# Kernel tuning notes

Measured on AMD Instinct MI355X. Metric: run time of the kernel, lower is better.

Reference implementation:

```python
import jax, jax.numpy as jnp
import numpy as np

NEG_SLOPE = 0.2  # GAT LeakyReLU slope
NEG_INF = -1e9


def setup_inputs() -> dict:
    key = jax.random.key(0)
    ks = jax.random.split(key, 5)
    B, N, D = 16, 1024, 256
    H, F = 4, 64  # heads, per-head out dim (out_dim=256)
    x = jax.random.normal(ks[0], (B, N, D), dtype=jnp.float32)
    adj = jax.random.uniform(ks[1], (B, N, N), dtype=jnp.float32)
    W = jax.random.normal(ks[2], (D, H * F), dtype=jnp.float32) * (1.0 / np.sqrt(D))
    a_src = jax.random.normal(ks[3], (H, F), dtype=jnp.float32) * (1.0 / np.sqrt(F))
    a_dst = jax.random.normal(ks[4], (H, F), dtype=jnp.float32) * (1.0 / np.sqrt(F))
    bias = jnp.zeros((H * F,), dtype=jnp.float32)
    return {"x": x, "adj": adj, "W": W, "a_src": a_src, "a_dst": a_dst, "bias": bias}


def reference(x, adj, W, a_src, a_dst, bias):
    B, N, D = x.shape
    H, F = a_src.shape
    # Linear transform per head: [B,N,H,F]
    h = jnp.einsum("bnd,dhf->bnhf", x, W.reshape(D, H, F))
    # Attention logit components: [B,N,H]
    e_src = jnp.einsum("bnhf,hf->bnh", h, a_src)
    e_dst = jnp.einsum("bnhf,hf->bnh", h, a_dst)
    # logits[b,i,j,h]: target i gathers from source j (edge = adj[b,i,j] > 0.5)
    logits = e_dst[:, :, None, :] + e_src[:, None, :, :]
    logits = jnp.where(logits >= 0, logits, NEG_SLOPE * logits)  # LeakyReLU
    mask = adj > 0.5  # [B,N,N]
    logits = jnp.where(mask[..., None], logits, NEG_INF)
    att = jax.nn.softmax(logits, axis=2)  # softmax over source neighbors j
    out = jnp.einsum("bijh,bjhf->bihf", att, h)  # aggregate
    return out.reshape(B, N, H * F) + bias  # concat heads
```

## Files before the change

### kernel.cpp

```cpp
#include <hip/hip_runtime.h>

typedef __bf16 bf16x8 __attribute__((ext_vector_type(8)));
typedef float f32x4 __attribute__((ext_vector_type(4)));

constexpr int Bsz = 16;
constexpr int Nsz = 1024;
constexpr int Dsz = 256;
constexpr int Hsz = 4;
constexpr int HFsz = 256;
constexpr int BN = Bsz * Nsz;
constexpr float LOG2E = 1.44269504088896340736f;

__device__ __forceinline__ unsigned f2bf(float f) {
    unsigned u = __float_as_uint(f);
    return (u + 0x7FFFu + ((u >> 16) & 1u)) >> 16;
}

__global__ __launch_bounds__(256) void wcvt(const float* __restrict__ Wm,
                                            unsigned short* __restrict__ WbT) {
    const int t = threadIdx.x;
    const int c = blockIdx.x * 4 + (t >> 6);
    const int d0 = (t & 63) * 4;
    const float v0 = Wm[(size_t)(d0 + 0) * HFsz + c];
    const float v1 = Wm[(size_t)(d0 + 1) * HFsz + c];
    const float v2 = Wm[(size_t)(d0 + 2) * HFsz + c];
    const float v3 = Wm[(size_t)(d0 + 3) * HFsz + c];
    uint2 pk;
    pk.x = f2bf(v0) | (f2bf(v1) << 16);
    pk.y = f2bf(v2) | (f2bf(v3) << 16);
    *(uint2*)&WbT[(size_t)c * Dsz + d0] = pk;
}

__global__ __launch_bounds__(256) void gat_h_e3(
    const float* __restrict__ x,
    const unsigned short* __restrict__ WbT,
    const float* __restrict__ a_src,
    const float* __restrict__ a_dst,
    unsigned short* __restrict__ hT,
    float* __restrict__ esrcT,
    float* __restrict__ edstT)
{
    const int n0g = blockIdx.x * 32, b = n0g >> 10, n0 = n0g & 1023;
    const int t = threadIdx.x, lane = t & 63, w = t >> 6;
    const int m = lane & 15, q = lane >> 4;

    __shared__ alignas(16) unsigned short Lds[4 * 64 * 40];

    const float4* x4 = (const float4*)(x + (size_t)n0g * Dsz);
#pragma unroll
    for (int i = 0; i < 8; ++i) {
        const int f = t + 256 * i;
        const int row = f >> 6, d4 = (f & 63) * 4;
        const float4 xv = x4[f];
        uint2 pk;
        pk.x = f2bf(xv.x) | (f2bf(xv.y) << 16);
        pk.y = f2bf(xv.z) | (f2bf(xv.w) << 16);
        *(uint2*)&Lds[row * 264 + d4] = pk;
    }
    __syncthreads();

    const unsigned short* Ab = WbT + (size_t)(w * 64 + m) * Dsz + q * 8;
    f32x4 acc[4][2];
#pragma unroll
    for (int ht = 0; ht < 4; ++ht)
#pragma unroll
        for (int nt = 0; nt < 2; ++nt) acc[ht][nt] = (f32x4){0.f, 0.f, 0.f, 0.f};

#pragma unroll
    for (int kk = 0; kk < 8; ++kk) {
        const int k0 = kk * 32;
        const bf16x8 bfr0 = *(const bf16x8*)&Lds[(0 * 16 + m) * 264 + k0 + q * 8];
        const bf16x8 bfr1 = *(const bf16x8*)&Lds[(1 * 16 + m) * 264 + k0 + q * 8];
#pragma unroll
        for (int ht = 0; ht < 4; ++ht) {
            const bf16x8 afr = *(const bf16x8*)&Ab[ht * 16 * Dsz + k0];
            acc[ht][0] = __builtin_amdgcn_mfma_f32_16x16x32_bf16(afr, bfr0, acc[ht][0], 0, 0, 0);
            acc[ht][1] = __builtin_amdgcn_mfma_f32_16x16x32_bf16(afr, bfr1, acc[ht][1], 0, 0, 0);
        }
    }

    float ps0 = 0.f, ps1 = 0.f, pd0 = 0.f, pd1 = 0.f;
#pragma unroll
    for (int ht = 0; ht < 4; ++ht)
#pragma unroll
        for (int r = 0; r < 4; ++r) {
            const float as = a_src[w * 64 + ht * 16 + q * 4 + r];
            const float ad = a_dst[w * 64 + ht * 16 + q * 4 + r];
            ps0 += acc[ht][0][r] * as;  ps1 += acc[ht][1][r] * as;
            pd0 += acc[ht][0][r] * ad;  pd1 += acc[ht][1][r] * ad;
        }
    ps0 += __shfl_xor(ps0, 16, 64); ps0 += __shfl_xor(ps0, 32, 64);
    ps1 += __shfl_xor(ps1, 16, 64); ps1 += __shfl_xor(ps1, 32, 64);
    pd0 += __shfl_xor(pd0, 16, 64); pd0 += __shfl_xor(pd0, 32, 64);
    pd1 += __shfl_xor(pd1, 16, 64); pd1 += __shfl_xor(pd1, 32, 64);
    if (q == 0) {
        const size_t eb = (size_t)(b * Hsz + w) * Nsz + n0;
        esrcT[eb + m]      = ps0 * LOG2E;  esrcT[eb + 16 + m] = ps1 * LOG2E;
        edstT[eb + m]      = pd0 * LOG2E;  edstT[eb + 16 + m] = pd1 * LOG2E;
    }

    __syncthreads();

#pragma unroll
    for (int ht = 0; ht < 4; ++ht)
#pragma unroll
        for (int r = 0; r < 4; ++r) {
            const int hf = ht * 16 + q * 4 + r;
            Lds[w * 2560 + hf * 40 + m]      = (unsigned short)f2bf(acc[ht][0][r]);
            Lds[w * 2560 + hf * 40 + 16 + m] = (unsigned short)f2bf(acc[ht][1][r]);
        }
#pragma unroll
    for (int s = 0; s < 4; ++s) {
        const int hf = s * 16 + (lane >> 2), ck = lane & 3;
        const bf16x8 hv = *(const bf16x8*)&Lds[w * 2560 + hf * 40 + ck * 8];
        *(bf16x8*)&hT[(size_t)(b * HFsz + w * 64 + hf) * Nsz + n0 + ck * 8] = hv;
    }
}

__device__ __forceinline__ unsigned pexp2(float ed, float e0, float e1,
                                          float a0, float a1) {
    float v0 = ed + e0, v1 = ed + e1;
    v0 = fmaxf(v0, 0.2f * v0);
    v1 = fmaxf(v1, 0.2f * v1);
    float p0, p1;
    asm("v_exp_f32 %0, %1" : "=v"(p0) : "v"(v0));
    asm("v_exp_f32 %0, %1" : "=v"(p1) : "v"(v1));
    unsigned u0 = __float_as_uint(p0), u1 = __float_as_uint(p1);
    u0 = (a0 > 0.5f) ? u0 : 0u;
    u1 = (a1 > 0.5f) ? u1 : 0u;
    return (u0 >> 16) | (u1 & 0xFFFF0000u);
}

__global__ __launch_bounds__(256, 6) void gat_attn6(
    const float* __restrict__ adj,
    const unsigned short* __restrict__ hT,
    const float* __restrict__ esrcT,
    const float* __restrict__ edstT,
    const float* __restrict__ bias,
    float* __restrict__ outp)
{
    const int gid = blockIdx.x;
    const int b  = gid & 15;
    const int hw = (gid >> 4) & 3;
    const int i0 = (gid >> 6) * 16;
    const int t = threadIdx.x;
    const int lane = t & 63, ws = t >> 6;
    const int m = lane & 15, q = lane >> 4;

    __shared__ alignas(16) float comb[4 * 64 * 20];

    const float* adjr = adj + (size_t)b * Nsz * Nsz + (size_t)(i0 + m) * Nsz;
    const float* esb  = esrcT + (size_t)(b * Hsz + hw) * Nsz;
    const float ed_s  = edstT[(size_t)(b * Hsz + hw) * Nsz + i0 + m];
    const unsigned short* hTb = hT + (size_t)(b * HFsz + hw * 64 + m) * Nsz + q * 8;

    bf16x8 ones;
#pragma unroll
    for (int i = 0; i < 8; ++i)
        ((unsigned short*)&ones)[i] = 0x3F80;

    f32x4 acc[4];
#pragma unroll
    for (int nt = 0; nt < 4; ++nt) acc[nt] = (f32x4){0.f, 0.f, 0.f, 0.f};
    f32x4 acc5 = (f32x4){0.f, 0.f, 0.f, 0.f};

#pragma unroll 1
    for (int jt = 0; jt < 4; ++jt) {
        const int j0 = (ws * 4 + jt) * 64;
#pragma unroll
        for (int kk = 0; kk < 2; ++kk) {
            const int jc = j0 + kk * 32 + q * 8;
            const float4 a0 = *(const float4*)&adjr[jc];
            const float4 a1 = *(const float4*)&adjr[jc + 4];
            const float4 e0 = *(const float4*)&esb[jc];
            const float4 e1 = *(const float4*)&esb[jc + 4];
            bf16x8 bfr[4];
#pragma unroll
            for (int nt = 0; nt < 4; ++nt)
                bfr[nt] = *(const bf16x8*)&hTb[(size_t)nt * 16 * Nsz + j0 + kk * 32];

            union { unsigned u[4]; bf16x8 v; } af;
            af.u[0] = pexp2(ed_s, e0.x, e0.y, a0.x, a0.y);
            af.u[1] = pexp2(ed_s, e0.z, e0.w, a0.z, a0.w);
            af.u[2] = pexp2(ed_s, e1.x, e1.y, a1.x, a1.y);
            af.u[3] = pexp2(ed_s, e1.z, e1.w, a1.z, a1.w);

#pragma unroll
            for (int nt = 0; nt < 4; ++nt)
                acc[nt] = __builtin_amdgcn_mfma_f32_16x16x32_bf16(
                    af.v, bfr[nt], acc[nt], 0, 0, 0);
            acc5 = __builtin_amdgcn_mfma_f32_16x16x32_bf16(af.v, ones, acc5,
                                                           0, 0, 0);
        }
    }

    __syncthreads();
    {
        float* cw = comb + (ws * 64 + lane) * 20;
#pragma unroll
        for (int nt = 0; nt < 4; ++nt)
#pragma unroll
            for (int r = 0; r < 4; ++r) cw[nt * 4 + r] = acc[nt][r];
#pragma unroll
        for (int r = 0; r < 4; ++r) cw[16 + r] = acc5[r];
    }
    __syncthreads();

    const int row = t >> 4, c4 = t & 15;
    const int rq = row >> 2, rr = row & 3;
    const int nt4 = (c4 >> 2) * 4;
    const int mb = (c4 & 3) * 4;
    float n0 = 0.f, n1 = 0.f, n2 = 0.f, n3 = 0.f, den = 0.f;
#pragma unroll
    for (int w4 = 0; w4 < 4; ++w4) {
        const float* cb = comb + (w4 * 64 + rq * 16) * 20;
        den += cb[16 + rr];
        n0 += cb[(mb + 0) * 20 + nt4 + rr];
        n1 += cb[(mb + 1) * 20 + nt4 + rr];
        n2 += cb[(mb + 2) * 20 + nt4 + rr];
        n3 += cb[(mb + 3) * 20 + nt4 + rr];
    }
    const float inv = 1.f / den;
    const float4 b4 = *(const float4*)&bias[hw * 64 + c4 * 4];
    float4 o;
    o.x = n0 * inv + b4.x;  o.y = n1 * inv + b4.y;
    o.z = n2 * inv + b4.z;  o.w = n3 * inv + b4.w;
    *(float4*)&outp[(size_t)(b * Nsz + i0 + row) * HFsz + hw * 64 + c4 * 4] = o;
}

extern "C" void kernel_launch(void* const* d_in, const int* in_sizes, int n_in,
                              void* d_out, int out_size, void* d_ws, size_t ws_size,
                              hipStream_t stream) {
    const float* x     = (const float*)d_in[0];
    const float* adj   = (const float*)d_in[1];
    const float* Wm    = (const float*)d_in[2];
    const float* a_src = (const float*)d_in[3];
    const float* a_dst = (const float*)d_in[4];
    const float* bias  = (const float*)d_in[5];
    float* outp = (float*)d_out;

    unsigned short* hT  = (unsigned short*)d_ws;
    unsigned short* WbT = hT + (size_t)BN * HFsz;
    float* esrcT = (float*)(WbT + (size_t)HFsz * Dsz);
    float* edstT = esrcT + (size_t)Bsz * Hsz * Nsz;

    wcvt<<<dim3(64), dim3(256), 0, stream>>>(Wm, WbT);
    gat_h_e3<<<dim3(BN / 32), dim3(256), 0, stream>>>(x, WbT, a_src, a_dst,
                                                      hT, esrcT, edstT);
    gat_attn6<<<dim3(4096), dim3(256), 0, stream>>>(adj, hT, esrcT, edstT,
                                                    bias, outp);
}
```

Before: 212.7 us.

## Share adjacency tiles across heads via double-buffered LDS in 512-thread blocks

Each block now covers all four heads for a 16-row tile, using 8 waves (4 heads by 2 j-halves) instead of one block per head. Adjacency rows are loaded once into double-buffered shared memory and reused by the four head waves, so adj traffic from global memory drops to a quarter. The cost is two barriers per j-tile, a larger LDS footprint and bigger blocks, which may lower occupancy and add synchronisation stalls.

```diff
diff --git a/kernel.cpp b/kernel.cpp
--- a/kernel.cpp
+++ b/kernel.cpp
@@ -131,7 +131,7 @@
     return (u0 >> 16) | (u1 & 0xFFFF0000u);
 }
 
-__global__ __launch_bounds__(256, 6) void gat_attn6(
+__global__ __launch_bounds__(512, 6) void gat_attn7(
     const float* __restrict__ adj,
     const unsigned short* __restrict__ hT,
     const float* __restrict__ esrcT,
@@ -141,18 +141,23 @@
 {
     const int gid = blockIdx.x;
     const int b  = gid & 15;
-    const int hw = (gid >> 4) & 3;
-    const int i0 = (gid >> 6) * 16;
+    const int i0 = (gid >> 4) * 16;
     const int t = threadIdx.x;
     const int lane = t & 63, ws = t >> 6;
+    const int hh = ws & 3, jh = ws >> 2;
     const int m = lane & 15, q = lane >> 4;
 
-    __shared__ alignas(16) float comb[4 * 64 * 20];
-
-    const float* adjr = adj + (size_t)b * Nsz * Nsz + (size_t)(i0 + m) * Nsz;
-    const float* esb  = esrcT + (size_t)(b * Hsz + hw) * Nsz;
-    const float ed_s  = edstT[(size_t)(b * Hsz + hw) * Nsz + i0 + m];
-    const unsigned short* hTb = hT + (size_t)(b * HFsz + hw * 64 + m) * Nsz + q * 8;
+    __shared__ alignas(16) float smem[10240];
+
+    const float* adjSg = adj + (size_t)b * Nsz * Nsz
+                             + (size_t)(i0 + hh * 4 + q) * Nsz + m * 4;
+    float* stW = &smem[(jh * 2) * 1088 + (hh * 4 + q) * 68 + m * 4];
+    const float* stR = &smem[(jh * 2) * 1088 + m * 68];
+
+    const float* esb = esrcT + (size_t)(b * Hsz + hh) * Nsz;
+    const float ed_s = edstT[(size_t)(b * Hsz + hh) * Nsz + i0 + m];
+    const unsigned short* hTb = hT + (size_t)(b * HFsz + hh * 64 + m) * Nsz + q * 8;
+    const int jt0 = jh * 8;
 
     bf16x8 ones;
 #pragma unroll
@@ -164,14 +169,26 @@
     for (int nt = 0; nt < 4; ++nt) acc[nt] = (f32x4){0.f, 0.f, 0.f, 0.f};
     f32x4 acc5 = (f32x4){0.f, 0.f, 0.f, 0.f};
 
+    {
+        const float4 g = *(const float4*)&adjSg[jt0 * 64];
+        *(float4*)&stW[0] = g;
+    }
+    __syncthreads();
+
 #pragma unroll 1
-    for (int jt = 0; jt < 4; ++jt) {
-        const int j0 = (ws * 4 + jt) * 64;
+    for (int jl = 0; jl < 8; ++jl) {
+        const int buf = jl & 1;
+        const int j0 = (jt0 + jl) * 64;
+
+        float4 g;
+        if (jl < 7) g = *(const float4*)&adjSg[(jt0 + jl + 1) * 64];
+
+        const float* rd = stR + buf * 1088;
 #pragma unroll
         for (int kk = 0; kk < 2; ++kk) {
             const int jc = j0 + kk * 32 + q * 8;
-            const float4 a0 = *(const float4*)&adjr[jc];
-            const float4 a1 = *(const float4*)&adjr[jc + 4];
+            const float4 a0 = *(const float4*)&rd[kk * 32 + q * 8];
+            const float4 a1 = *(const float4*)&rd[kk * 32 + q * 8 + 4];
             const float4 e0 = *(const float4*)&esb[jc];
             const float4 e1 = *(const float4*)&esb[jc + 4];
             bf16x8 bfr[4];
@@ -192,11 +209,14 @@
             acc5 = __builtin_amdgcn_mfma_f32_16x16x32_bf16(af.v, ones, acc5,
                                                            0, 0, 0);
         }
-    }
-
-    __syncthreads();
+
+        __syncthreads();
+        if (jl < 7) *(float4*)&stW[(buf ^ 1) * 1088] = g;
+        __syncthreads();
+    }
+
     {
-        float* cw = comb + (ws * 64 + lane) * 20;
+        float* cw = &smem[t * 20];
 #pragma unroll
         for (int nt = 0; nt < 4; ++nt)
 #pragma unroll
@@ -206,26 +226,30 @@
     }
     __syncthreads();
 
-    const int row = t >> 4, c4 = t & 15;
-    const int rq = row >> 2, rr = row & 3;
-    const int nt4 = (c4 >> 2) * 4;
-    const int mb = (c4 & 3) * 4;
-    float n0 = 0.f, n1 = 0.f, n2 = 0.f, n3 = 0.f, den = 0.f;
-#pragma unroll
-    for (int w4 = 0; w4 < 4; ++w4) {
-        const float* cb = comb + (w4 * 64 + rq * 16) * 20;
-        den += cb[16 + rr];
-        n0 += cb[(mb + 0) * 20 + nt4 + rr];
-        n1 += cb[(mb + 1) * 20 + nt4 + rr];
-        n2 += cb[(mb + 2) * 20 + nt4 + rr];
-        n3 += cb[(mb + 3) * 20 + nt4 + rr];
-    }
-    const float inv = 1.f / den;
-    const float4 b4 = *(const float4*)&bias[hw * 64 + c4 * 4];
-    float4 o;
-    o.x = n0 * inv + b4.x;  o.y = n1 * inv + b4.y;
-    o.z = n2 * inv + b4.z;  o.w = n3 * inv + b4.w;
-    *(float4*)&outp[(size_t)(b * Nsz + i0 + row) * HFsz + hw * 64 + c4 * 4] = o;
+#pragma unroll
+    for (int u = 0; u < 2; ++u) {
+        const int idx = t * 2 + u;
+        const int row = idx >> 6, c4g = idx & 63;
+        const int hh2 = c4g >> 4, c4l = c4g & 15;
+        const int rq = row >> 2, rr = row & 3;
+        const int nt4 = (c4l >> 2) * 4, mb = (c4l & 3) * 4;
+        float n0 = 0.f, n1 = 0.f, n2 = 0.f, n3 = 0.f, den = 0.f;
+#pragma unroll
+        for (int j2 = 0; j2 < 2; ++j2) {
+            const float* cb = &smem[((j2 * 4 + hh2) * 64 + rq * 16) * 20];
+            den += cb[16 + rr];
+            n0 += cb[(mb + 0) * 20 + nt4 + rr];
+            n1 += cb[(mb + 1) * 20 + nt4 + rr];
+            n2 += cb[(mb + 2) * 20 + nt4 + rr];
+            n3 += cb[(mb + 3) * 20 + nt4 + rr];
+        }
+        const float inv = 1.f / den;
+        const float4 b4 = *(const float4*)&bias[hh2 * 64 + c4l * 4];
+        float4 o;
+        o.x = n0 * inv + b4.x;  o.y = n1 * inv + b4.y;
+        o.z = n2 * inv + b4.z;  o.w = n3 * inv + b4.w;
+        *(float4*)&outp[(size_t)(b * Nsz + i0 + row) * HFsz + c4g * 4] = o;
+    }
 }
 
 extern "C" void kernel_launch(void* const* d_in, const int* in_sizes, int n_in,
@@ -247,6 +271,6 @@
     wcvt<<<dim3(64), dim3(256), 0, stream>>>(Wm, WbT);
     gat_h_e3<<<dim3(BN / 32), dim3(256), 0, stream>>>(x, WbT, a_src, a_dst,
                                                       hT, esrcT, edstT);
-    gat_attn6<<<dim3(4096), dim3(256), 0, stream>>>(adj, hT, esrcT, edstT,
+    gat_attn7<<<dim3(1024), dim3(512), 0, stream>>>(adj, hT, esrcT, edstT,
                                                     bias, outp);
 }
```

Measured after the change: 195.1 us. 8.3% less time.
